# Kernel optimization log

Hardware: AMD Instinct MI355X
Metric: run time of the kernel (lower is better)

The kernel has to match this reference:

```python
import jax, jax.numpy as jnp
import numpy as np


def rational_hat(points, centers, radius):
    # points: [B, P, 2], centers: [K, 2], radius: [1]
    # L1 distance of each point to each center: [B, P, K]
    norm = jnp.abs(points[:, :, None, :] - centers[None, None, :, :]).sum(-1)
    r = jnp.abs(radius[0])
    val = 1.0 / (1.0 + norm) - 1.0 / (1.0 + jnp.abs(r - norm))
    return val.sum(axis=1)  # [B, K]


def setup_inputs() -> dict:
    key = jax.random.key(0)
    k1, k2, k3, k4, k5 = jax.random.split(key, 5)
    B, N0, N1, N2, K = 32, 20000, 10000, 10000, 64
    return {
        "beta_0_up": jax.random.uniform(k1, (B, N0, 2), dtype=jnp.float32),
        "beta_0_down": jax.random.uniform(k2, (B, N0, 2), dtype=jnp.float32),
        "beta0_ext": jax.random.uniform(k3, (B, N1, 2), dtype=jnp.float32),
        "beta1_ext": jax.random.uniform(k4, (B, N2, 2), dtype=jnp.float32),
        "centers": jax.random.uniform(k5, (K, 2), dtype=jnp.float32),
        "radius": jnp.full((1,), 0.1, dtype=jnp.float32),
    }


def reference(beta_0_up, beta_0_down, beta0_ext, beta1_ext, centers, radius):
    x0, y0 = beta0_ext[..., 0], beta0_ext[..., 1]
    x1, y1 = beta1_ext[..., 0], beta1_ext[..., 1]
    b0_1st = jnp.stack([x0, 1.0 - x0], axis=-1)  # [B, N1, 2]
    b0_2nd = jnp.stack([y0, 1.0 - y0], axis=-1)
    b1_1st = jnp.stack([x1, 1.0 - x1], axis=-1)  # [B, N2, 2]
    b1_2nd = jnp.stack([y1, 1.0 - y1], axis=-1)
    ph_down = jnp.concatenate([beta_0_down, b0_1st, b1_1st], axis=1)  # [B, P, 2]
    ph_up = jnp.concatenate([beta_0_up, b0_2nd, b1_2nd], axis=1)
    up_out = rational_hat(ph_up, centers, radius)    # [B, K]
    down_out = rational_hat(ph_down, centers, radius)
    tpl = -((up_out - down_out) ** 2).sum()
    x = jnp.concatenate([up_out, down_out], axis=1)  # [B, 2K]
    return (x, tpl)
```

## Files before the change

### kernel.cpp

```cpp
#include <hip/hip_runtime.h>

typedef float v2f __attribute__((ext_vector_type(2)));

#define NB 32
#define N0 20000
#define N1 10000
#define N2 10000
#define NT_A 157
#define KC_A 8
#define KC_B 16
#define NBINS 4096
#define SENT 3.0e4f

__global__ __launch_bounds__(256, 8) void hat_kernel(
    const float* __restrict__ up0, const float* __restrict__ down0,
    const float* __restrict__ ext0, const float* __restrict__ ext1,
    const float* __restrict__ centers, const float* __restrict__ radius,
    float* __restrict__ out)
{
    const int tid  = threadIdx.x;
    const int lane = tid & 63;
    const int wave = tid >> 6;
    const float r  = fabsf(radius[0]);

    __shared__ unsigned hist[NBINS];
    __shared__ float    red[4 * KC_B];

    if (blockIdx.x < 256) {
        const int id   = blockIdx.x;
        const int cc   = id & 3;
        const int side = (id >> 2) & 1;
        const int b    = id >> 3;
        const int cbase = cc * KC_B;

        for (int j = tid; j < NBINS; j += 256) hist[j] = 0;
        __syncthreads();

        const float2* e0 = (const float2*)(ext0 + (size_t)b * (N1*2));
        const float2* e1 = (const float2*)(ext1 + (size_t)b * (N2*2));
        for (int i = tid; i < N1; i += 256) {
            const float2 q0 = e0[i];
            const float2 q1 = e1[i];
            const float vv0 = (side == 0) ? q0.y : q0.x;
            const float vv1 = (side == 0) ? q1.y : q1.x;
            int b0 = (int)(vv0 * (float)NBINS);
            int b1 = (int)(vv1 * (float)NBINS);
            b0 = min(max(b0, 0), NBINS - 1);
            b1 = min(max(b1, 0), NBINS - 1);
            atomicAdd(&hist[b0], 1u);
            atomicAdd(&hist[b1], 1u);
        }
        __syncthreads();

        float Ak[KC_B], mk[KC_B];
        #pragma unroll
        for (int k = 0; k < KC_B; ++k) {
            const float cx = centers[2*(cbase+k)];
            const float cy = centers[2*(cbase+k)+1];
            Ak[k] = fabsf(1.0f - (cx + cy));
            mk[k] = 0.5f * (1.0f + (cx - cy));
        }

        float part[KC_B];
        #pragma unroll
        for (int k = 0; k < KC_B; ++k) part[k] = 0.f;

        #pragma unroll
        for (int jj = 0; jj < NBINS/256; ++jj) {
            const int j = jj*256 + tid;
            const float cntf = (float)hist[j];
            const float vvj  = ((float)j + 0.5f) * (1.0f/(float)NBINS);
            #pragma unroll
            for (int k = 0; k < KC_B; ++k) {
                const float s  = vvj - mk[k];
                const float tt = fmaxf(Ak[k], 2.0f*fabsf(s));
                const float d1 = 1.0f + tt;
                const float rn = r - tt;
                const float d2 = 1.0f + fabsf(rn);
                const float rc = __builtin_amdgcn_rcpf(d1 * d2);
                part[k] = fmaf(cntf * (d2 - d1), rc, part[k]);
            }
        }

        {
            #pragma unroll
            for (int k = 0; k < 8; ++k) {
                const bool hi = lane & 32;
                const float send = hi ? part[k]   : part[k+8];
                const float keep = hi ? part[k+8] : part[k];
                part[k] = keep + __shfl_xor(send, 32, 64);
            }
            #pragma unroll
            for (int k = 0; k < 4; ++k) {
                const bool hi = lane & 16;
                const float send = hi ? part[k]   : part[k+4];
                const float keep = hi ? part[k+4] : part[k];
                part[k] = keep + __shfl_xor(send, 16, 64);
            }
            #pragma unroll
            for (int k = 0; k < 2; ++k) {
                const bool hi = lane & 8;
                const float send = hi ? part[k]   : part[k+2];
                const float keep = hi ? part[k+2] : part[k];
                part[k] = keep + __shfl_xor(send, 8, 64);
            }
            {
                const bool hi = lane & 4;
                const float send = hi ? part[0] : part[1];
                const float keep = hi ? part[1] : part[0];
                part[0] = keep + __shfl_xor(send, 4, 64);
            }
            part[0] += __shfl_xor(part[0], 2, 64);
            part[0] += __shfl_xor(part[0], 1, 64);
        }
        if ((lane & 3) == 0) red[wave * KC_B + (lane >> 2)] = part[0];
        __syncthreads();
        if (tid < KC_B) {
            const float s = red[tid] + red[KC_B + tid] + red[2*KC_B + tid] + red[3*KC_B + tid];
            atomicAdd(&out[b*128 + side*64 + cbase + tid], s);
        }
        return;
    }

    const int bid    = blockIdx.x - 256;
    const int tchunk = bid & 3;
    const int cc     = (bid >> 2) & 7;
    const int side   = (bid >> 5) & 1;
    const int b      = bid >> 6;
    const int cbase  = cc * KC_A;

    v2f nuc[KC_A], nvc[KC_A];
    #pragma unroll
    for (int k = 0; k < KC_A; ++k) {
        const float cx = centers[2*(cbase+k)];
        const float cy = centers[2*(cbase+k)+1];
        nuc[k] = (v2f){-(cx + cy), -(cx + cy)};
        nvc[k] = (v2f){-(cx - cy), -(cx - cy)};
    }

    const float4* base0 = (const float4*)((side == 0 ? up0 : down0) + (size_t)b * (N0*2));

    v2f acc[KC_A];
    #pragma unroll
    for (int k = 0; k < KC_A; ++k) acc[k] = (v2f){0.f, 0.f};
    const v2f one2 = (v2f){1.f, 1.f};

    for (int t = tchunk*4 + wave; t < NT_A; t += 16) {
        const int i = t*64 + lane;
        v2f u_, v_;
        if (i < N0/2) {
            const float4 q = base0[i];
            u_ = (v2f){q.x + q.y, q.z + q.w};
            v_ = (v2f){q.x - q.y, q.z - q.w};
        } else {
            u_ = (v2f){SENT, SENT};
            v_ = (v2f){0.f, 0.f};
        }

        #pragma unroll
        for (int k = 0; k < KC_A; ++k) {
            const v2f du = u_ + nuc[k];
            const v2f dv = v_ + nvc[k];
            const float tt0 = fmaxf(fabsf(du.x), fabsf(dv.x));
            const float tt1 = fmaxf(fabsf(du.y), fabsf(dv.y));
            const v2f tt = (v2f){tt0, tt1};
            const v2f d1 = tt + one2;
            const float rn0 = r - tt0;
            const float rn1 = r - tt1;
            const v2f d2 = (v2f){1.f + fabsf(rn0), 1.f + fabsf(rn1)};
            const v2f dd  = d1 * d2;
            const v2f num = d2 - d1;
            const v2f rc  = (v2f){__builtin_amdgcn_rcpf(dd.x),
                                  __builtin_amdgcn_rcpf(dd.y)};
            acc[k] = __builtin_elementwise_fma(num, rc, acc[k]);
        }
    }

    float a1[KC_A];
    #pragma unroll
    for (int k = 0; k < KC_A; ++k) a1[k] = acc[k].x + acc[k].y;

    {
        #pragma unroll
        for (int k = 0; k < 4; ++k) {
            const bool hi = lane & 32;
            const float send = hi ? a1[k]   : a1[k+4];
            const float keep = hi ? a1[k+4] : a1[k];
            a1[k] = keep + __shfl_xor(send, 32, 64);
        }
        #pragma unroll
        for (int k = 0; k < 2; ++k) {
            const bool hi = lane & 16;
            const float send = hi ? a1[k]   : a1[k+2];
            const float keep = hi ? a1[k+2] : a1[k];
            a1[k] = keep + __shfl_xor(send, 16, 64);
        }
        {
            const bool hi = lane & 8;
            const float send = hi ? a1[0] : a1[1];
            const float keep = hi ? a1[1] : a1[0];
            a1[0] = keep + __shfl_xor(send, 8, 64);
        }
        a1[0] += __shfl_xor(a1[0], 4, 64);
        a1[0] += __shfl_xor(a1[0], 2, 64);
        a1[0] += __shfl_xor(a1[0], 1, 64);
    }
    if ((lane & 7) == 0) red[wave * KC_A + (lane >> 3)] = a1[0];
    __syncthreads();
    if (tid < KC_A) {
        const float s = red[tid] + red[KC_A + tid] + red[2*KC_A + tid] + red[3*KC_A + tid];
        atomicAdd(&out[b*128 + side*64 + cbase + tid], s);
    }
}

__global__ __launch_bounds__(256) void tpl_kernel(float* __restrict__ out)
{
    __shared__ float red[256];
    float s = 0.f;
    for (int i = threadIdx.x; i < NB*64; i += 256) {
        const int b = i >> 6, k = i & 63;
        const float d = out[b*128 + k] - out[b*128 + 64 + k];
        s = fmaf(d, d, s);
    }
    red[threadIdx.x] = s;
    __syncthreads();
    for (int w = 128; w > 0; w >>= 1) {
        if (threadIdx.x < w) red[threadIdx.x] += red[threadIdx.x + w];
        __syncthreads();
    }
    if (threadIdx.x == 0) out[NB*128] = -red[0];
}

extern "C" void kernel_launch(void* const* d_in, const int* in_sizes, int n_in,
                              void* d_out, int out_size, void* d_ws, size_t ws_size,
                              hipStream_t stream) {
    const float* up0     = (const float*)d_in[0];
    const float* down0   = (const float*)d_in[1];
    const float* ext0    = (const float*)d_in[2];
    const float* ext1    = (const float*)d_in[3];
    const float* centers = (const float*)d_in[4];
    const float* radius  = (const float*)d_in[5];
    float* out = (float*)d_out;

    hipMemsetAsync(out, 0, NB * 128 * sizeof(float), stream);

    hat_kernel<<<dim3(256 + 2048), dim3(256), 0, stream>>>(
        up0, down0, ext0, ext1, centers, radius, out);
    tpl_kernel<<<1, 256, 0, stream>>>(out);
}
```

Measured before the change: 107.2 us.

## Interleave histogram blocks with direct blocks and split centers across waves

Places the histogram blocks at every eighth block slot so they are spread across the grid instead of all launching first. In the direct-distance path each wave now owns its own group of 8 centers and walks a strided set of 64-point tiles, so the four waves in a block load the same points and may share them through cache. The grid shrinks from 2304 to 2048 blocks. Each wave now issues its own global atomicAdd in place of the shared-memory cross-wave reduction and barrier, which means more global atomics per output element.

After: 140.4 us. 1.31x slower.

```diff
diff --git a/kernel.cpp b/kernel.cpp
--- a/kernel.cpp
+++ b/kernel.cpp
@@ -7,6 +7,7 @@
 #define N1 10000
 #define N2 10000
 #define NT_A 157
+#define T_A 14
 #define KC_A 8
 #define KC_B 16
 #define NBINS 4096
@@ -26,8 +27,10 @@
     __shared__ unsigned hist[NBINS];
     __shared__ float    red[4 * KC_B];
 
-    if (blockIdx.x < 256) {
-        const int id   = blockIdx.x;
+    const int slot = blockIdx.x;
+
+    if ((slot & 7) == 0) {
+        const int id   = slot >> 3;
         const int cc   = id & 3;
         const int side = (id >> 2) & 1;
         const int b    = id >> 3;
@@ -122,12 +125,14 @@
         return;
     }
 
-    const int bid    = blockIdx.x - 256;
-    const int tchunk = bid & 3;
-    const int cc     = (bid >> 2) & 7;
-    const int side   = (bid >> 5) & 1;
-    const int b      = bid >> 6;
-    const int cbase  = cc * KC_A;
+    const int aid    = slot - (slot >> 3) - 1;
+    const int half   = aid & 1;
+    const int rest0  = aid >> 1;
+    const int tchunk = rest0 % T_A;
+    const int rest1  = rest0 / T_A;
+    const int side   = rest1 & 1;
+    const int b      = rest1 >> 1;
+    const int cbase  = (half * 4 + wave) * KC_A;
 
     v2f nuc[KC_A], nvc[KC_A];
     #pragma unroll
@@ -145,7 +150,7 @@
     for (int k = 0; k < KC_A; ++k) acc[k] = (v2f){0.f, 0.f};
     const v2f one2 = (v2f){1.f, 1.f};
 
-    for (int t = tchunk*4 + wave; t < NT_A; t += 16) {
+    for (int t = tchunk; t < NT_A; t += T_A) {
         const int i = t*64 + lane;
         v2f u_, v_;
         if (i < N0/2) {
@@ -205,11 +210,8 @@
         a1[0] += __shfl_xor(a1[0], 2, 64);
         a1[0] += __shfl_xor(a1[0], 1, 64);
     }
-    if ((lane & 7) == 0) red[wave * KC_A + (lane >> 3)] = a1[0];
-    __syncthreads();
-    if (tid < KC_A) {
-        const float s = red[tid] + red[KC_A + tid] + red[2*KC_A + tid] + red[3*KC_A + tid];
-        atomicAdd(&out[b*128 + side*64 + cbase + tid], s);
+    if ((lane & 7) == 0) {
+        atomicAdd(&out[b*128 + side*64 + cbase + (lane >> 3)], a1[0]);
     }
 }
 
@@ -244,7 +246,7 @@
 
     hipMemsetAsync(out, 0, NB * 128 * sizeof(float), stream);
 
-    hat_kernel<<<dim3(256 + 2048), dim3(256), 0, stream>>>(
+    hat_kernel<<<dim3(2048), dim3(256), 0, stream>>>(
         up0, down0, ext0, ext1, centers, radius, out);
     tpl_kernel<<<1, 256, 0, stream>>>(out);
 }
```
